# Kernel tuning notes

Hardware: AMD Instinct MI355X
Metric: run time of the kernel (lower is better)

Reference implementation:

```python
import jax, jax.numpy as jnp
import numpy as np
import math

B, S, DM, H = 2, 2048, 1024, 16
HD = DM // H  # head_dim = 64


def setup_inputs() -> dict:
    key = jax.random.key(0)
    ks = jax.random.split(key, 7)
    mk = lambda k, shp, s=1.0: jax.random.normal(k, shp, dtype=jnp.float32) * s
    return {
        "q": mk(ks[0], (B, S, DM)),
        "k": mk(ks[1], (B, S, DM)),
        "v": mk(ks[2], (B, S, DM)),
        "wq": mk(ks[3], (DM, DM), 0.02),
        "wk": mk(ks[4], (DM, DM), 0.02),
        "wv": mk(ks[5], (DM, DM), 0.02),
        "wo": mk(ks[6], (DM, DM), 0.02),
    }


def reference(q, k, v, wq, wk, wv, wo):
    bsz, seqlen, _ = q.shape
    # bias-free linear projections: y = x @ W.T (torch nn.Linear layout [out,in])
    def proj(x, w):
        y = jnp.einsum('bsd,ed->bse', x, w)
        return y.reshape(bsz, seqlen, H, HD).transpose(0, 2, 1, 3)  # (B,H,S,HD)
    xq, xk, xv = proj(q, wq), proj(k, wk), proj(v, wv)
    scores = jnp.einsum('bhqd,bhkd->bhqk', xq, xk) / math.sqrt(HD)  # (B,H,S,S)
    # causal mask: -inf above the diagonal
    causal = jnp.tril(jnp.ones((seqlen, seqlen), dtype=bool))
    scores = jnp.where(causal[None, None], scores, -jnp.inf)
    probs = jax.nn.softmax(scores.astype(jnp.float32), axis=-1).astype(xq.dtype)
    # dropout p=0.0 -> identity in eval / p=0 config
    out = jnp.einsum('bhqk,bhkd->bhqd', probs, xv)  # (B,H,S,HD)
    out = out.transpose(0, 2, 1, 3).reshape(bsz, seqlen, DM)
    return jnp.einsum('bsd,ed->bse', out, wo)
```

## Files before the change

kernel.cpp:

```cpp
#include <hip/hip_runtime.h>
#include <hip/hip_bf16.h>
#include <stdint.h>

#define NB 2
#define NS 2048
#define NDM 1024
#define NH 16
#define NHD 64
#define NTOK (NB * NS)

typedef __bf16 bf16x8 __attribute__((ext_vector_type(8)));
typedef float f32x4 __attribute__((ext_vector_type(4)));
typedef uint16_t u16x8 __attribute__((ext_vector_type(8)));

static __device__ __forceinline__ uint16_t f2bf(float f) {
  __bf16 b = (__bf16)f;
  union { __bf16 b; uint16_t u; } x; x.b = b;
  return x.u;
}

static __device__ __forceinline__ u16x8 cvt8(float4 a, float4 b) {
  u16x8 v;
  v[0] = f2bf(a.x); v[1] = f2bf(a.y); v[2] = f2bf(a.z); v[3] = f2bf(a.w);
  v[4] = f2bf(b.x); v[5] = f2bf(b.y); v[6] = f2bf(b.z); v[7] = f2bf(b.w);
  return v;
}

static __device__ __forceinline__ void gload_lds16(const void* g, void* l) {
  __builtin_amdgcn_global_load_lds(
      (const __attribute__((address_space(1))) void*)g,
      (__attribute__((address_space(3))) void*)l, 16, 0, 0);
}

__global__ __launch_bounds__(256) void cvt_w(
    const float* __restrict__ w0, const float* __restrict__ w1,
    const float* __restrict__ w2, const float* __restrict__ w3,
    uint16_t* __restrict__ o0, uint16_t* __restrict__ o1,
    uint16_t* __restrict__ o2, uint16_t* __restrict__ o3) {
  int y = blockIdx.y;
  const float* src = (y == 0) ? w0 : (y == 1) ? w1 : (y == 2) ? w2 : w3;
  uint16_t* dst = (y == 0) ? o0 : (y == 1) ? o1 : (y == 2) ? o2 : o3;
  int i = ((int)blockIdx.x * 256 + (int)threadIdx.x) * 8;
  float4 a = *(const float4*)(src + i);
  float4 b = *(const float4*)(src + i + 4);
  *(u16x8*)&dst[i] = cvt8(a, b);
}

__global__ __launch_bounds__(256) void cvt_x(
    const float* __restrict__ x0, const float* __restrict__ x1,
    const float* __restrict__ x2, uint16_t* __restrict__ o0,
    uint16_t* __restrict__ o1, uint16_t* __restrict__ o2) {
  int y = blockIdx.y;
  const float* src = (y == 0) ? x0 : (y == 1) ? x1 : x2;
  uint16_t* dst = (y == 0) ? o0 : (y == 1) ? o1 : o2;
  int i = ((int)blockIdx.x * 256 + (int)threadIdx.x) * 8;
  float4 a = *(const float4*)(src + i);
  float4 b = *(const float4*)(src + i + 4);
  *(u16x8*)&dst[i] = cvt8(a, b);
}

__global__ __launch_bounds__(256) void proj_gemm(
    const uint16_t* __restrict__ xbq, const uint16_t* __restrict__ xbk,
    const uint16_t* __restrict__ xbv, const uint16_t* __restrict__ wqb,
    const uint16_t* __restrict__ wkb, const uint16_t* __restrict__ wvb,
    uint16_t* __restrict__ XQ, uint16_t* __restrict__ XK,
    uint16_t* __restrict__ XVT) {
  __shared__ uint16_t As[2][128][64];
  __shared__ uint16_t Bs[2][128][64];
  int z = blockIdx.z;
  const uint16_t* A = (z == 0) ? xbq : (z == 1) ? xbk : xbv;
  const uint16_t* W = (z == 0) ? wqb : (z == 1) ? wkb : wvb;
  int m0 = blockIdx.x * 128, n0 = blockIdx.y * 128;
  int tid = threadIdx.x;
  int lane = tid & 63, w = tid >> 6;
  int g = lane >> 4, r16 = lane & 15;
  int wm = w >> 1, wn = w & 1;
  int bce = ((lane & 7) ^ ((lane >> 3) & 7)) * 8;
  int brlane = lane >> 3;

  f32x4 acc[4][4] = {};

  #pragma unroll
  for (int i = 0; i < 4; ++i) {
    int row = w * 32 + i * 8;
    gload_lds16(A + (size_t)(m0 + row + brlane) * NDM + bce, &As[0][row][0]);
    gload_lds16(W + (size_t)(n0 + row + brlane) * NDM + bce, &Bs[0][row][0]);
  }
  __syncthreads();

  for (int t = 0; t < 16; ++t) {
    int cur = t & 1, nxt = cur ^ 1;
    if (t < 15) {
      int k1 = (t + 1) * 64;
      #pragma unroll
      for (int i = 0; i < 4; ++i) {
        int row = w * 32 + i * 8;
        gload_lds16(A + (size_t)(m0 + row + brlane) * NDM + k1 + bce,
                    &As[nxt][row][0]);
        gload_lds16(W + (size_t)(n0 + row + brlane) * NDM + k1 + bce,
                    &Bs[nxt][row][0]);
      }
    }

    #pragma unroll
    for (int kc = 0; kc < 2; ++kc) {
      bf16x8 af[4], bf[4];
      #pragma unroll
      for (int i = 0; i < 4; ++i) {
        int gran = (kc * 4 + g) ^ (r16 & 7);
        af[i] = *(const bf16x8*)&As[cur][wm * 64 + i * 16 + r16][gran * 8];
        bf[i] = *(const bf16x8*)&Bs[cur][wn * 64 + i * 16 + r16][gran * 8];
      }
      #pragma unroll
      for (int mi = 0; mi < 4; ++mi)
        #pragma unroll
        for (int ni = 0; ni < 4; ++ni)
          acc[mi][ni] = __builtin_amdgcn_mfma_f32_16x16x32_bf16(
              af[mi], bf[ni], acc[mi][ni], 0, 0, 0);
    }
    __syncthreads();
  }

  float scale = (z == 0) ? 0.125f * 1.44269504088896340736f : 1.0f;
  #pragma unroll
  for (int mi = 0; mi < 4; ++mi) {
    #pragma unroll
    for (int ni = 0; ni < 4; ++ni) {
      int m = m0 + wm * 64 + mi * 16 + g * 4;
      int n = n0 + wn * 64 + ni * 16 + r16;
      f32x4 a = acc[mi][ni];
      if (z == 2) {
        ushort4 pk;
        pk.x = f2bf(a[0]); pk.y = f2bf(a[1]);
        pk.z = f2bf(a[2]); pk.w = f2bf(a[3]);
        *(ushort4*)&XVT[(size_t)n * NTOK + m] = pk;
      } else {
        uint16_t* Y = (z == 0) ? XQ : XK;
        #pragma unroll
        for (int j = 0; j < 4; ++j)
          Y[(size_t)(m + j) * NDM + n] = f2bf(a[j] * scale);
      }
    }
  }
}

__global__ __launch_bounds__(256) void attn_kernel(
    const uint16_t* __restrict__ XQ, const uint16_t* __restrict__ XK,
    const uint16_t* __restrict__ XVT, uint16_t* __restrict__ AO) {
  __shared__ uint16_t Klds[64][72];
  __shared__ uint16_t Vlds[64][72];
  __shared__ uint16_t Plds[4][16][72];

  int tid = threadIdx.x;
  int lane = tid & 63;
  int w = tid >> 6;
  int g = lane >> 4, r16 = lane & 15;
  int srow = tid >> 2;
  int scol = (tid & 3) * 16;

  int item = (int)blockIdx.x;
  int qc = 31 - (item >> 5);
  int bh = item & 31;
  int b = bh >> 4, h = bh & 15;
  int q0 = qc * 64;
  int q0w = q0 + w * 16;
  int T = qc + 1;

  const uint16_t* qb =
      XQ + (size_t)(b * NS + q0w + r16) * NDM + h * NHD + g * 8;
  bf16x8 qf0 = *(const bf16x8*)qb;
  bf16x8 qf1 = *(const bf16x8*)(qb + 32);

  f32x4 oacc[4] = {};
  float mrow = -1e30f, lsum = 0.f;

  const uint16_t* kbase = XK + (size_t)(b * NS + srow) * NDM + h * NHD + scol;
  const uint16_t* vbase = XVT + (size_t)(h * NHD + srow) * NTOK + b * NS + scol;

  u16x8 kr0 = *(const u16x8*)(kbase);
  u16x8 kr1 = *(const u16x8*)(kbase + 8);
  u16x8 vr0 = *(const u16x8*)(vbase);
  u16x8 vr1 = *(const u16x8*)(vbase + 8);

  for (int t = 0; t < T; ++t) {
    int kv0 = t * 64;
    __syncthreads();
    *(u16x8*)&Klds[srow][scol]     = kr0;
    *(u16x8*)&Klds[srow][scol + 8] = kr1;
    *(u16x8*)&Vlds[srow][scol]     = vr0;
    *(u16x8*)&Vlds[srow][scol + 8] = vr1;
    __syncthreads();
    if (t + 1 < T) {
      const uint16_t* kp = kbase + (size_t)(t + 1) * 64 * NDM;
      const uint16_t* vp = vbase + (t + 1) * 64;
      kr0 = *(const u16x8*)(kp);
      kr1 = *(const u16x8*)(kp + 8);
      vr0 = *(const u16x8*)(vp);
      vr1 = *(const u16x8*)(vp + 8);
    }

    f32x4 sc[4];
    __builtin_amdgcn_s_setprio(1);
    #pragma unroll
    for (int t4 = 0; t4 < 4; ++t4) {
      bf16x8 kf0 = *(const bf16x8*)&Klds[t4 * 16 + r16][g * 8];
      bf16x8 kf1 = *(const bf16x8*)&Klds[t4 * 16 + r16][32 + g * 8];
      f32x4 x = __builtin_amdgcn_mfma_f32_16x16x32_bf16(
          kf0, qf0, (f32x4){0.f, 0.f, 0.f, 0.f}, 0, 0, 0);
      x = __builtin_amdgcn_mfma_f32_16x16x32_bf16(kf1, qf1, x, 0, 0, 0);
      sc[t4] = x;
    }
    __builtin_amdgcn_s_setprio(0);

    #pragma unroll
    for (int t4 = 0; t4 < 4; ++t4) {
      if (kv0 + t4 * 16 + 15 > q0w) {
        #pragma unroll
        for (int j = 0; j < 4; ++j)
          if (kv0 + t4 * 16 + g * 4 + j > q0w + r16) sc[t4][j] = -1e30f;
      }
    }

    float m16 = fmaxf(
        fmaxf(fmaxf(fmaxf(sc[0][0], sc[0][1]), fmaxf(sc[0][2], sc[0][3])),
              fmaxf(fmaxf(sc[1][0], sc[1][1]), fmaxf(sc[1][2], sc[1][3]))),
        fmaxf(fmaxf(fmaxf(sc[2][0], sc[2][1]), fmaxf(sc[2][2], sc[2][3])),
              fmaxf(fmaxf(sc[3][0], sc[3][1]), fmaxf(sc[3][2], sc[3][3]))));
    m16 = fmaxf(m16, __shfl_xor(m16, 16));
    m16 = fmaxf(m16, __shfl_xor(m16, 32));

    if (!__all(m16 <= mrow + 8.0f)) {
      float mnew = fmaxf(mrow, m16);
      float sf = __builtin_amdgcn_exp2f(mrow - mnew);
      mrow = mnew;
      lsum *= sf;
      #pragma unroll
      for (int j = 0; j < 4; ++j) {
        float sfj = __shfl(sf, g * 4 + j);
        #pragma unroll
        for (int dt = 0; dt < 4; ++dt) oacc[dt][j] *= sfj;
      }
    }

    #pragma unroll
    for (int t4 = 0; t4 < 4; ++t4) {
      float p0 = __builtin_amdgcn_exp2f(sc[t4][0] - mrow);
      float p1 = __builtin_amdgcn_exp2f(sc[t4][1] - mrow);
      float p2 = __builtin_amdgcn_exp2f(sc[t4][2] - mrow);
      float p3 = __builtin_amdgcn_exp2f(sc[t4][3] - mrow);
      lsum += (p0 + p1) + (p2 + p3);
      ushort4 pk;
      pk.x = f2bf(p0); pk.y = f2bf(p1); pk.z = f2bf(p2); pk.w = f2bf(p3);
      *(ushort4*)&Plds[w][r16][t4 * 16 + g * 4] = pk;
    }

    bf16x8 pa0 = *(const bf16x8*)&Plds[w][r16][g * 8];
    bf16x8 pa1 = *(const bf16x8*)&Plds[w][r16][32 + g * 8];
    __builtin_amdgcn_s_setprio(1);
    #pragma unroll
    for (int dt = 0; dt < 4; ++dt) {
      bf16x8 vf0 = *(const bf16x8*)&Vlds[dt * 16 + r16][g * 8];
      bf16x8 vf1 = *(const bf16x8*)&Vlds[dt * 16 + r16][32 + g * 8];
      oacc[dt] = __builtin_amdgcn_mfma_f32_16x16x32_bf16(pa0, vf0, oacc[dt], 0, 0, 0);
      oacc[dt] = __builtin_amdgcn_mfma_f32_16x16x32_bf16(pa1, vf1, oacc[dt], 0, 0, 0);
    }
    __builtin_amdgcn_s_setprio(0);
  }

  float l2 = lsum + __shfl_xor(lsum, 16);
  float ltot = l2 + __shfl_xor(l2, 32);
  #pragma unroll
  for (int j = 0; j < 4; ++j) {
    float lt = __shfl(ltot, g * 4 + j);
    float inv = 1.0f / lt;
    size_t ro = (size_t)(b * NS + q0 + w * 16 + g * 4 + j) * NDM + h * NHD;
    #pragma unroll
    for (int dt = 0; dt < 4; ++dt)
      AO[ro + dt * 16 + r16] = f2bf(oacc[dt][j] * inv);
  }
}

__global__ __launch_bounds__(256) void out_gemm(
    const uint16_t* __restrict__ AO, const uint16_t* __restrict__ wob,
    float* __restrict__ out) {
  __shared__ uint16_t As[2][128][64];
  __shared__ uint16_t Bs[2][128][64];
  int m0 = blockIdx.x * 128, n0 = blockIdx.y * 128;
  int tid = threadIdx.x;
  int lane = tid & 63, w = tid >> 6;
  int g = lane >> 4, r16 = lane & 15;
  int wm = w >> 1, wn = w & 1;
  int bce = ((lane & 7) ^ ((lane >> 3) & 7)) * 8;
  int brlane = lane >> 3;

  f32x4 acc[4][4] = {};

  #pragma unroll
  for (int i = 0; i < 4; ++i) {
    int row = w * 32 + i * 8;
    gload_lds16(AO + (size_t)(m0 + row + brlane) * NDM + bce, &As[0][row][0]);
    gload_lds16(wob + (size_t)(n0 + row + brlane) * NDM + bce, &Bs[0][row][0]);
  }
  __syncthreads();

  for (int t = 0; t < 16; ++t) {
    int cur = t & 1, nxt = cur ^ 1;
    if (t < 15) {
      int k1 = (t + 1) * 64;
      #pragma unroll
      for (int i = 0; i < 4; ++i) {
        int row = w * 32 + i * 8;
        gload_lds16(AO + (size_t)(m0 + row + brlane) * NDM + k1 + bce,
                    &As[nxt][row][0]);
        gload_lds16(wob + (size_t)(n0 + row + brlane) * NDM + k1 + bce,
                    &Bs[nxt][row][0]);
      }
    }

    #pragma unroll
    for (int kc = 0; kc < 2; ++kc) {
      bf16x8 af[4], bf[4];
      #pragma unroll
      for (int i = 0; i < 4; ++i) {
        int gran = (kc * 4 + g) ^ (r16 & 7);
        af[i] = *(const bf16x8*)&As[cur][wm * 64 + i * 16 + r16][gran * 8];
        bf[i] = *(const bf16x8*)&Bs[cur][wn * 64 + i * 16 + r16][gran * 8];
      }
      #pragma unroll
      for (int mi = 0; mi < 4; ++mi)
        #pragma unroll
        for (int ni = 0; ni < 4; ++ni)
          acc[mi][ni] = __builtin_amdgcn_mfma_f32_16x16x32_bf16(
              af[mi], bf[ni], acc[mi][ni], 0, 0, 0);
    }
    __syncthreads();
  }

  #pragma unroll
  for (int mi = 0; mi < 4; ++mi) {
    #pragma unroll
    for (int ni = 0; ni < 4; ++ni) {
      int m = m0 + wm * 64 + mi * 16 + g * 4;
      int n = n0 + wn * 64 + ni * 16 + r16;
      #pragma unroll
      for (int j = 0; j < 4; ++j)
        out[(size_t)(m + j) * NDM + n] = acc[mi][ni][j];
    }
  }
}

extern "C" void kernel_launch(void* const* d_in, const int* in_sizes, int n_in,
                              void* d_out, int out_size, void* d_ws,
                              size_t ws_size, hipStream_t stream) {
  const float* q  = (const float*)d_in[0];
  const float* k  = (const float*)d_in[1];
  const float* v  = (const float*)d_in[2];
  const float* wq = (const float*)d_in[3];
  const float* wk = (const float*)d_in[4];
  const float* wv = (const float*)d_in[5];
  const float* wo = (const float*)d_in[6];

  const size_t XN = (size_t)NTOK * NDM;
  const size_t WN = (size_t)NDM * NDM;
  uint16_t* XQ  = (uint16_t*)d_ws;
  uint16_t* XK  = XQ + XN;
  uint16_t* XVT = XK + XN;
  uint16_t* WQB = XVT + XN;
  uint16_t* WKB = WQB + WN;
  uint16_t* WVB = WKB + WN;
  uint16_t* WOB = WVB + WN;
  uint16_t* XBQ = WOB + WN;
  uint16_t* XBK = XBQ + XN;
  uint16_t* XBV = XBK + XN;
  uint16_t* AO  = XBQ;

  cvt_w<<<dim3(WN / (256 * 8), 4), 256, 0, stream>>>(
      wq, wk, wv, wo, WQB, WKB, WVB, WOB);
  cvt_x<<<dim3(XN / (256 * 8), 3), 256, 0, stream>>>(
      q, k, v, XBQ, XBK, XBV);
  proj_gemm<<<dim3(NTOK / 128, NDM / 128, 3), 256, 0, stream>>>(
      XBQ, XBK, XBV, WQB, WKB, WVB, XQ, XK, XVT);
  attn_kernel<<<dim3(1024), 256, 0, stream>>>(XQ, XK, XVT, AO);
  out_gemm<<<dim3(NTOK / 128, NDM / 128), 256, 0, stream>>>(
      AO, WOB, (float*)d_out);
}
```

Measured before the change: 128.2 us.

## Pair causal attention work items per block and stage V-transpose store through LDS

The attention kernel now launches 512 blocks, each processing two query chunks, a long one (item i) and a short one (item 1023-i), so every block gets roughly equal causal work instead of relying on the hardware scheduler to balance 1024 uneven blocks. Separately, the V projection epilogue writes its transposed tile into shared memory with a swizzle and then emits coalesced 16-byte rows to XVT, replacing scattered 8-byte transposed global stores. The pairing reduces the number of resident blocks and serializes two items per block, which may cut parallelism on a large GPU. The LDS staging adds a barrier plus extra shared-memory traffic.

After: 117.9 us. 1.09x faster.

```diff
diff --git a/kernel.cpp b/kernel.cpp
--- a/kernel.cpp
+++ b/kernel.cpp
@@ -65,8 +65,7 @@
     const uint16_t* __restrict__ wkb, const uint16_t* __restrict__ wvb,
     uint16_t* __restrict__ XQ, uint16_t* __restrict__ XK,
     uint16_t* __restrict__ XVT) {
-  __shared__ uint16_t As[2][128][64];
-  __shared__ uint16_t Bs[2][128][64];
+  __shared__ uint16_t SM[2][2][128][64];
   int z = blockIdx.z;
   const uint16_t* A = (z == 0) ? xbq : (z == 1) ? xbk : xbv;
   const uint16_t* W = (z == 0) ? wqb : (z == 1) ? wkb : wvb;
@@ -83,8 +82,8 @@
   #pragma unroll
   for (int i = 0; i < 4; ++i) {
     int row = w * 32 + i * 8;
-    gload_lds16(A + (size_t)(m0 + row + brlane) * NDM + bce, &As[0][row][0]);
-    gload_lds16(W + (size_t)(n0 + row + brlane) * NDM + bce, &Bs[0][row][0]);
+    gload_lds16(A + (size_t)(m0 + row + brlane) * NDM + bce, &SM[0][0][row][0]);
+    gload_lds16(W + (size_t)(n0 + row + brlane) * NDM + bce, &SM[0][1][row][0]);
   }
   __syncthreads();
 
@@ -96,9 +95,9 @@
       for (int i = 0; i < 4; ++i) {
         int row = w * 32 + i * 8;
         gload_lds16(A + (size_t)(m0 + row + brlane) * NDM + k1 + bce,
-                    &As[nxt][row][0]);
+                    &SM[nxt][0][row][0]);
         gload_lds16(W + (size_t)(n0 + row + brlane) * NDM + k1 + bce,
-                    &Bs[nxt][row][0]);
+                    &SM[nxt][1][row][0]);
       }
     }
 
@@ -108,8 +107,8 @@
       #pragma unroll
       for (int i = 0; i < 4; ++i) {
         int gran = (kc * 4 + g) ^ (r16 & 7);
-        af[i] = *(const bf16x8*)&As[cur][wm * 64 + i * 16 + r16][gran * 8];
-        bf[i] = *(const bf16x8*)&Bs[cur][wn * 64 + i * 16 + r16][gran * 8];
+        af[i] = *(const bf16x8*)&SM[cur][0][wm * 64 + i * 16 + r16][gran * 8];
+        bf[i] = *(const bf16x8*)&SM[cur][1][wn * 64 + i * 16 + r16][gran * 8];
       }
       #pragma unroll
       for (int mi = 0; mi < 4; ++mi)
@@ -121,21 +120,40 @@
     __syncthreads();
   }
 
-  float scale = (z == 0) ? 0.125f * 1.44269504088896340736f : 1.0f;
-  #pragma unroll
-  for (int mi = 0; mi < 4; ++mi) {
-    #pragma unroll
-    for (int ni = 0; ni < 4; ++ni) {
-      int m = m0 + wm * 64 + mi * 16 + g * 4;
-      int n = n0 + wn * 64 + ni * 16 + r16;
-      f32x4 a = acc[mi][ni];
-      if (z == 2) {
+  if (z == 2) {
+    uint16_t* T = &SM[0][0][0][0];
+    #pragma unroll
+    for (int mi = 0; mi < 4; ++mi) {
+      #pragma unroll
+      for (int ni = 0; ni < 4; ++ni) {
+        int tr = wn * 64 + ni * 16 + r16;
+        int tc = wm * 64 + mi * 16 + g * 4;
+        int gran = tc >> 3, sub = g & 1;
+        f32x4 a = acc[mi][ni];
         ushort4 pk;
         pk.x = f2bf(a[0]); pk.y = f2bf(a[1]);
         pk.z = f2bf(a[2]); pk.w = f2bf(a[3]);
-        *(ushort4*)&XVT[(size_t)n * NTOK + m] = pk;
-      } else {
-        uint16_t* Y = (z == 0) ? XQ : XK;
+        *(ushort4*)(T + tr * 128 + ((gran ^ (tr & 7)) << 3) + (sub << 2)) = pk;
+      }
+    }
+    __syncthreads();
+    #pragma unroll
+    for (int it = 0; it < 8; ++it) {
+      int row = it * 16 + (tid >> 4);
+      int grn = tid & 15;
+      u16x8 vv = *(const u16x8*)(T + row * 128 + ((grn ^ (row & 7)) << 3));
+      *(u16x8*)&XVT[(size_t)(n0 + row) * NTOK + m0 + grn * 8] = vv;
+    }
+  } else {
+    float scale = (z == 0) ? 0.125f * 1.44269504088896340736f : 1.0f;
+    uint16_t* Y = (z == 0) ? XQ : XK;
+    #pragma unroll
+    for (int mi = 0; mi < 4; ++mi) {
+      #pragma unroll
+      for (int ni = 0; ni < 4; ++ni) {
+        int m = m0 + wm * 64 + mi * 16 + g * 4;
+        int n = n0 + wn * 64 + ni * 16 + r16;
+        f32x4 a = acc[mi][ni];
         #pragma unroll
         for (int j = 0; j < 4; ++j)
           Y[(size_t)(m + j) * NDM + n] = f2bf(a[j] * scale);
@@ -158,125 +176,129 @@
   int srow = tid >> 2;
   int scol = (tid & 3) * 16;
 
-  int item = (int)blockIdx.x;
-  int qc = 31 - (item >> 5);
-  int bh = item & 31;
-  int b = bh >> 4, h = bh & 15;
-  int q0 = qc * 64;
-  int q0w = q0 + w * 16;
-  int T = qc + 1;
-
-  const uint16_t* qb =
-      XQ + (size_t)(b * NS + q0w + r16) * NDM + h * NHD + g * 8;
-  bf16x8 qf0 = *(const bf16x8*)qb;
-  bf16x8 qf1 = *(const bf16x8*)(qb + 32);
-
-  f32x4 oacc[4] = {};
-  float mrow = -1e30f, lsum = 0.f;
-
-  const uint16_t* kbase = XK + (size_t)(b * NS + srow) * NDM + h * NHD + scol;
-  const uint16_t* vbase = XVT + (size_t)(h * NHD + srow) * NTOK + b * NS + scol;
-
-  u16x8 kr0 = *(const u16x8*)(kbase);
-  u16x8 kr1 = *(const u16x8*)(kbase + 8);
-  u16x8 vr0 = *(const u16x8*)(vbase);
-  u16x8 vr1 = *(const u16x8*)(vbase + 8);
-
-  for (int t = 0; t < T; ++t) {
-    int kv0 = t * 64;
-    __syncthreads();
-    *(u16x8*)&Klds[srow][scol]     = kr0;
-    *(u16x8*)&Klds[srow][scol + 8] = kr1;
-    *(u16x8*)&Vlds[srow][scol]     = vr0;
-    *(u16x8*)&Vlds[srow][scol + 8] = vr1;
-    __syncthreads();
-    if (t + 1 < T) {
-      const uint16_t* kp = kbase + (size_t)(t + 1) * 64 * NDM;
-      const uint16_t* vp = vbase + (t + 1) * 64;
-      kr0 = *(const u16x8*)(kp);
-      kr1 = *(const u16x8*)(kp + 8);
-      vr0 = *(const u16x8*)(vp);
-      vr1 = *(const u16x8*)(vp + 8);
-    }
-
-    f32x4 sc[4];
-    __builtin_amdgcn_s_setprio(1);
-    #pragma unroll
-    for (int t4 = 0; t4 < 4; ++t4) {
-      bf16x8 kf0 = *(const bf16x8*)&Klds[t4 * 16 + r16][g * 8];
-      bf16x8 kf1 = *(const bf16x8*)&Klds[t4 * 16 + r16][32 + g * 8];
-      f32x4 x = __builtin_amdgcn_mfma_f32_16x16x32_bf16(
-          kf0, qf0, (f32x4){0.f, 0.f, 0.f, 0.f}, 0, 0, 0);
-      x = __builtin_amdgcn_mfma_f32_16x16x32_bf16(kf1, qf1, x, 0, 0, 0);
-      sc[t4] = x;
-    }
-    __builtin_amdgcn_s_setprio(0);
-
-    #pragma unroll
-    for (int t4 = 0; t4 < 4; ++t4) {
-      if (kv0 + t4 * 16 + 15 > q0w) {
+  for (int which = 0; which < 2; ++which) {
+    int item = (which == 0) ? (int)blockIdx.x : (1023 - (int)blockIdx.x);
+    int qc = 31 - (item >> 5);
+    int bh = item & 31;
+    int b = bh >> 4, h = bh & 15;
+    int q0 = qc * 64;
+    int q0w = q0 + w * 16;
+    int T = qc + 1;
+
+    const uint16_t* qb =
+        XQ + (size_t)(b * NS + q0w + r16) * NDM + h * NHD + g * 8;
+    bf16x8 qf0 = *(const bf16x8*)qb;
+    bf16x8 qf1 = *(const bf16x8*)(qb + 32);
+
+    f32x4 oacc[4] = {};
+    float mrow = -1e30f, lsum = 0.f;
+
+    const uint16_t* kbase =
+        XK + (size_t)(b * NS + srow) * NDM + h * NHD + scol;
+    const uint16_t* vbase =
+        XVT + (size_t)(h * NHD + srow) * NTOK + b * NS + scol;
+
+    u16x8 kr0 = *(const u16x8*)(kbase);
+    u16x8 kr1 = *(const u16x8*)(kbase + 8);
+    u16x8 vr0 = *(const u16x8*)(vbase);
+    u16x8 vr1 = *(const u16x8*)(vbase + 8);
+
+    for (int t = 0; t < T; ++t) {
+      int kv0 = t * 64;
+      __syncthreads();
+      *(u16x8*)&Klds[srow][scol]     = kr0;
+      *(u16x8*)&Klds[srow][scol + 8] = kr1;
+      *(u16x8*)&Vlds[srow][scol]     = vr0;
+      *(u16x8*)&Vlds[srow][scol + 8] = vr1;
+      __syncthreads();
+      if (t + 1 < T) {
+        const uint16_t* kp = kbase + (size_t)(t + 1) * 64 * NDM;
+        const uint16_t* vp = vbase + (t + 1) * 64;
+        kr0 = *(const u16x8*)(kp);
+        kr1 = *(const u16x8*)(kp + 8);
+        vr0 = *(const u16x8*)(vp);
+        vr1 = *(const u16x8*)(vp + 8);
+      }
+
+      f32x4 sc[4];
+      __builtin_amdgcn_s_setprio(1);
+      #pragma unroll
+      for (int t4 = 0; t4 < 4; ++t4) {
+        bf16x8 kf0 = *(const bf16x8*)&Klds[t4 * 16 + r16][g * 8];
+        bf16x8 kf1 = *(const bf16x8*)&Klds[t4 * 16 + r16][32 + g * 8];
+        f32x4 x = __builtin_amdgcn_mfma_f32_16x16x32_bf16(
+            kf0, qf0, (f32x4){0.f, 0.f, 0.f, 0.f}, 0, 0, 0);
+        x = __builtin_amdgcn_mfma_f32_16x16x32_bf16(kf1, qf1, x, 0, 0, 0);
+        sc[t4] = x;
+      }
+      __builtin_amdgcn_s_setprio(0);
+
+      #pragma unroll
+      for (int t4 = 0; t4 < 4; ++t4) {
+        if (kv0 + t4 * 16 + 15 > q0w) {
+          #pragma unroll
+          for (int j = 0; j < 4; ++j)
+            if (kv0 + t4 * 16 + g * 4 + j > q0w + r16) sc[t4][j] = -1e30f;
+        }
+      }
+
+      float m16 = fmaxf(
+          fmaxf(fmaxf(fmaxf(sc[0][0], sc[0][1]), fmaxf(sc[0][2], sc[0][3])),
+                fmaxf(fmaxf(sc[1][0], sc[1][1]), fmaxf(sc[1][2], sc[1][3]))),
+          fmaxf(fmaxf(fmaxf(sc[2][0], sc[2][1]), fmaxf(sc[2][2], sc[2][3])),
+                fmaxf(fmaxf(sc[3][0], sc[3][1]), fmaxf(sc[3][2], sc[3][3]))));
+      m16 = fmaxf(m16, __shfl_xor(m16, 16));
+      m16 = fmaxf(m16, __shfl_xor(m16, 32));
+
+      if (!__all(m16 <= mrow + 8.0f)) {
+        float mnew = fmaxf(mrow, m16);
+        float sf = __builtin_amdgcn_exp2f(mrow - mnew);
+        mrow = mnew;
+        lsum *= sf;
         #pragma unroll
-        for (int j = 0; j < 4; ++j)
-          if (kv0 + t4 * 16 + g * 4 + j > q0w + r16) sc[t4][j] = -1e30f;
-      }
-    }
-
-    float m16 = fmaxf(
-        fmaxf(fmaxf(fmaxf(sc[0][0], sc[0][1]), fmaxf(sc[0][2], sc[0][3])),
-              fmaxf(fmaxf(sc[1][0], sc[1][1]), fmaxf(sc[1][2], sc[1][3]))),
-        fmaxf(fmaxf(fmaxf(sc[2][0], sc[2][1]), fmaxf(sc[2][2], sc[2][3])),
-              fmaxf(fmaxf(sc[3][0], sc[3][1]), fmaxf(sc[3][2], sc[3][3]))));
-    m16 = fmaxf(m16, __shfl_xor(m16, 16));
-    m16 = fmaxf(m16, __shfl_xor(m16, 32));
-
-    if (!__all(m16 <= mrow + 8.0f)) {
-      float mnew = fmaxf(mrow, m16);
-      float sf = __builtin_amdgcn_exp2f(mrow - mnew);
-      mrow = mnew;
-      lsum *= sf;
-      #pragma unroll
-      for (int j = 0; j < 4; ++j) {
-        float sfj = __shfl(sf, g * 4 + j);
-        #pragma unroll
-        for (int dt = 0; dt < 4; ++dt) oacc[dt][j] *= sfj;
-      }
-    }
-
-    #pragma unroll
-    for (int t4 = 0; t4 < 4; ++t4) {
-      float p0 = __builtin_amdgcn_exp2f(sc[t4][0] - mrow);
-      float p1 = __builtin_amdgcn_exp2f(sc[t4][1] - mrow);
-      float p2 = __builtin_amdgcn_exp2f(sc[t4][2] - mrow);
-      float p3 = __builtin_amdgcn_exp2f(sc[t4][3] - mrow);
-      lsum += (p0 + p1) + (p2 + p3);
-      ushort4 pk;
-      pk.x = f2bf(p0); pk.y = f2bf(p1); pk.z = f2bf(p2); pk.w = f2bf(p3);
-      *(ushort4*)&Plds[w][r16][t4 * 16 + g * 4] = pk;
-    }
-
-    bf16x8 pa0 = *(const bf16x8*)&Plds[w][r16][g * 8];
-    bf16x8 pa1 = *(const bf16x8*)&Plds[w][r16][32 + g * 8];
-    __builtin_amdgcn_s_setprio(1);
-    #pragma unroll
-    for (int dt = 0; dt < 4; ++dt) {
-      bf16x8 vf0 = *(const bf16x8*)&Vlds[dt * 16 + r16][g * 8];
-      bf16x8 vf1 = *(const bf16x8*)&Vlds[dt * 16 + r16][32 + g * 8];
-      oacc[dt] = __builtin_amdgcn_mfma_f32_16x16x32_bf16(pa0, vf0, oacc[dt], 0, 0, 0);
-      oacc[dt] = __builtin_amdgcn_mfma_f32_16x16x32_bf16(pa1, vf1, oacc[dt], 0, 0, 0);
-    }
-    __builtin_amdgcn_s_setprio(0);
-  }
-
-  float l2 = lsum + __shfl_xor(lsum, 16);
-  float ltot = l2 + __shfl_xor(l2, 32);
-  #pragma unroll
-  for (int j = 0; j < 4; ++j) {
-    float lt = __shfl(ltot, g * 4 + j);
-    float inv = 1.0f / lt;
-    size_t ro = (size_t)(b * NS + q0 + w * 16 + g * 4 + j) * NDM + h * NHD;
-    #pragma unroll
-    for (int dt = 0; dt < 4; ++dt)
-      AO[ro + dt * 16 + r16] = f2bf(oacc[dt][j] * inv);
+        for (int j = 0; j < 4; ++j) {
+          float sfj = __shfl(sf, g * 4 + j);
+          #pragma unroll
+          for (int dt = 0; dt < 4; ++dt) oacc[dt][j] *= sfj;
+        }
+      }
+
+      #pragma unroll
+      for (int t4 = 0; t4 < 4; ++t4) {
+        float p0 = __builtin_amdgcn_exp2f(sc[t4][0] - mrow);
+        float p1 = __builtin_amdgcn_exp2f(sc[t4][1] - mrow);
+        float p2 = __builtin_amdgcn_exp2f(sc[t4][2] - mrow);
+        float p3 = __builtin_amdgcn_exp2f(sc[t4][3] - mrow);
+        lsum += (p0 + p1) + (p2 + p3);
+        ushort4 pk;
+        pk.x = f2bf(p0); pk.y = f2bf(p1); pk.z = f2bf(p2); pk.w = f2bf(p3);
+        *(ushort4*)&Plds[w][r16][t4 * 16 + g * 4] = pk;
+      }
+
+      bf16x8 pa0 = *(const bf16x8*)&Plds[w][r16][g * 8];
+      bf16x8 pa1 = *(const bf16x8*)&Plds[w][r16][32 + g * 8];
+      __builtin_amdgcn_s_setprio(1);
+      #pragma unroll
+      for (int dt = 0; dt < 4; ++dt) {
+        bf16x8 vf0 = *(const bf16x8*)&Vlds[dt * 16 + r16][g * 8];
+        bf16x8 vf1 = *(const bf16x8*)&Vlds[dt * 16 + r16][32 + g * 8];
+        oacc[dt] = __builtin_amdgcn_mfma_f32_16x16x32_bf16(pa0, vf0, oacc[dt], 0, 0, 0);
+        oacc[dt] = __builtin_amdgcn_mfma_f32_16x16x32_bf16(pa1, vf1, oacc[dt], 0, 0, 0);
+      }
+      __builtin_amdgcn_s_setprio(0);
+    }
+
+    float l2 = lsum + __shfl_xor(lsum, 16);
+    float ltot = l2 + __shfl_xor(l2, 32);
+    #pragma unroll
+    for (int j = 0; j < 4; ++j) {
+      float lt = __shfl(ltot, g * 4 + j);
+      float inv = 1.0f / lt;
+      size_t ro = (size_t)(b * NS + q0 + w * 16 + g * 4 + j) * NDM + h * NHD;
+      #pragma unroll
+      for (int dt = 0; dt < 4; ++dt)
+        AO[ro + dt * 16 + r16] = f2bf(oacc[dt][j] * inv);
+    }
   }
 }
 
@@ -380,7 +402,7 @@
       q, k, v, XBQ, XBK, XBV);
   proj_gemm<<<dim3(NTOK / 128, NDM / 128, 3), 256, 0, stream>>>(
       XBQ, XBK, XBV, WQB, WKB, WVB, XQ, XK, XVT);
-  attn_kernel<<<dim3(1024), 256, 0, stream>>>(XQ, XK, XVT, AO);
+  attn_kernel<<<dim3(512), 256, 0, stream>>>(XQ, XK, XVT, AO);
   out_gemm<<<dim3(NTOK / 128, NDM / 128), 256, 0, stream>>>(
       AO, WOB, (float*)d_out);
 }
```
